# Kernel optimization log

Measured on AMD Instinct MI355X. Metric: run time of the kernel, lower is better.

## Reference

```python
import jax, jax.numpy as jnp
import numpy as np

L, H, D, V, TMAX = 6, 16, 1024, 32000, 2048
HD = D // H
EPS = 1e-5


def _ln(x, g, b):
    m = jnp.mean(x, axis=-1, keepdims=True)
    v = jnp.var(x, axis=-1, keepdims=True)
    return (x - m) * jax.lax.rsqrt(v + EPS) * g + b


def setup_inputs() -> dict:
    key = jax.random.key(0)
    ks = jax.random.split(key, 16)
    s = 0.02
    inp = {
        'idx': jax.random.randint(ks[0], (2, TMAX), 0, V),
        'targets': jax.random.randint(ks[1], (2, TMAX), 0, V),
        'tok_emb': jax.random.normal(ks[2], (V, D), jnp.float32) * s,
        'pos_emb': jax.random.normal(ks[3], (TMAX, D), jnp.float32) * s,
        'wq': jax.random.normal(ks[4], (L, D, D), jnp.float32) * s,
        'wk': jax.random.normal(ks[5], (L, D, D), jnp.float32) * s,
        'wv': jax.random.normal(ks[6], (L, D, D), jnp.float32) * s,
        'w_proj': jax.random.normal(ks[7], (L, D, D), jnp.float32) * s,
        'b_proj': jnp.zeros((L, D), jnp.float32),
        'w_fc1': jax.random.normal(ks[8], (L, D, 4 * D), jnp.float32) * s,
        'b_fc1': jnp.zeros((L, 4 * D), jnp.float32),
        'w_fc2': jax.random.normal(ks[9], (L, 4 * D, D), jnp.float32) * s,
        'b_fc2': jnp.zeros((L, D), jnp.float32),
        'ln1_g': jnp.ones((L, D), jnp.float32), 'ln1_b': jnp.zeros((L, D), jnp.float32),
        'ln2_g': jnp.ones((L, D), jnp.float32), 'ln2_b': jnp.zeros((L, D), jnp.float32),
        'lnf_g': jnp.ones((D,), jnp.float32), 'lnf_b': jnp.zeros((D,), jnp.float32),
        'w_head': jax.random.normal(ks[10], (D, V), jnp.float32) * s,
        'b_head': jnp.zeros((V,), jnp.float32),
    }
    return inp


def reference(idx, targets, tok_emb, pos_emb, wq, wk, wv, w_proj, b_proj,
              w_fc1, b_fc1, w_fc2, b_fc2, ln1_g, ln1_b, ln2_g, ln2_b,
              lnf_g, lnf_b, w_head, b_head):
    B, T = idx.shape
    x = tok_emb[idx] + pos_emb[:T]  # [B,T,D]
    causal = jnp.tril(jnp.ones((T, T), bool))
    scale = HD ** -0.5
    for l in range(L):
        h = _ln(x, ln1_g[l], ln1_b[l])
        q = (h @ wq[l]).reshape(B, T, H, HD)
        k = (h @ wk[l]).reshape(B, T, H, HD)
        v = (h @ wv[l]).reshape(B, T, H, HD)
        att = jnp.einsum('bqhd,bkhd->bhqk', q, k) * scale
        att = jnp.where(causal, att, -jnp.inf)
        att = jax.nn.softmax(att, axis=-1)  # dropout is identity in eval
        o = jnp.einsum('bhqk,bkhd->bqhd', att, v).reshape(B, T, D)
        x = x + o @ w_proj[l] + b_proj[l]
        h = _ln(x, ln2_g[l], ln2_b[l])
        x = x + jax.nn.relu(h @ w_fc1[l] + b_fc1[l]) @ w_fc2[l] + b_fc2[l]
    x = _ln(x, lnf_g, lnf_b)
    logits = x @ w_head + b_head  # [B,T,V]
    logp = jax.nn.log_softmax(logits, axis=-1)
    nll = -jnp.take_along_axis(logp, targets[..., None], axis=-1)[..., 0]
    loss = jnp.mean(nll)
    return logits, loss
```

## Files before the change

### kernel.cpp

```cpp
#include <hip/hip_runtime.h>

#define LAYERS 6
#define NH 16
#define DIM 1024
#define VOCAB 32000
#define SEQ 2048
#define NBATCH 2
#define HEADD 64
#define NROW (NBATCH*SEQ)
#define FF 4096
#define QKVS 3072
#define NCB (VOCAB/256)
#define LN_EPS 1e-5f

typedef unsigned short bfu;
typedef __attribute__((ext_vector_type(8))) short s16x8;
typedef __attribute__((ext_vector_type(4))) float f32x4;

__device__ __forceinline__ float bf2f(bfu u) { return __uint_as_float(((unsigned)u) << 16); }
__device__ __forceinline__ bfu f2bf(float x) {
  unsigned u = __float_as_uint(x);
  return (bfu)((u + 0x7fffu + ((u >> 16) & 1u)) >> 16);
}

__device__ __forceinline__ void gload16(const void* g, void* l) {
  __builtin_amdgcn_global_load_lds((const __attribute__((address_space(1))) void*)g,
                                   (__attribute__((address_space(3))) void*)l, 16, 0, 0);
}

__device__ __forceinline__ f32x4 mfma32(s16x8 a, s16x8 b, f32x4 c) {
  return __builtin_amdgcn_mfma_f32_16x16x32_bf16(a, b, c, 0, 0, 0);
}

__global__ __launch_bounds__(256) void tkernel(const float* __restrict__ in,
                                               bfu* __restrict__ out, int R, int C) {
  __shared__ bfu tile[32][33];
  int tx = threadIdx.x, ty = threadIdx.y;
  int bx = blockIdx.x * 32, by = blockIdx.y * 32;
#pragma unroll
  for (int i = 0; i < 4; ++i)
    tile[ty + i * 8][tx] = f2bf(in[(size_t)(by + ty + i * 8) * C + bx + tx]);
  __syncthreads();
#pragma unroll
  for (int i = 0; i < 4; ++i)
    out[(size_t)(bx + ty + i * 8) * R + by + tx] = tile[tx][ty + i * 8];
}

__global__ __launch_bounds__(256) void wtrans_kernel(const float* __restrict__ wq,
                                                     const float* __restrict__ wk,
                                                     const float* __restrict__ wv,
                                                     const float* __restrict__ wp,
                                                     const float* __restrict__ w1,
                                                     const float* __restrict__ w2,
                                                     bfu* __restrict__ qkvT,
                                                     bfu* __restrict__ wpT,
                                                     bfu* __restrict__ f1T,
                                                     bfu* __restrict__ f2T) {
  __shared__ bfu tile[32][33];
  int bi = blockIdx.x;
  const float* in; bfu* out; int R, C, id;
  if (bi < 4096) {
    int p = bi >> 10; id = bi & 1023;
    in = p == 0 ? wq : p == 1 ? wk : p == 2 ? wv : wp;
    out = (p == 3) ? wpT : qkvT + (size_t)p * DIM * DIM;
    R = DIM; C = DIM;
  } else if (bi < 8192) {
    id = bi - 4096; in = w1; out = f1T; R = DIM; C = FF;
  } else {
    id = bi - 8192; in = w2; out = f2T; R = FF; C = DIM;
  }
  int nbx = C >> 5;
  int bx = (id % nbx) * 32, by = (id / nbx) * 32;
  int tx = threadIdx.x, ty = threadIdx.y;
#pragma unroll
  for (int i = 0; i < 4; ++i)
    tile[ty + i * 8][tx] = f2bf(in[(size_t)(by + ty + i * 8) * C + bx + tx]);
  __syncthreads();
#pragma unroll
  for (int i = 0; i < 4; ++i)
    out[(size_t)(bx + ty + i * 8) * R + by + tx] = tile[tx][ty + i * 8];
}

__global__ __launch_bounds__(256) void vtrans_kernel(const bfu* __restrict__ qkvb,
                                                     bfu* __restrict__ vT) {
  __shared__ bfu tile[32][33];
  int bh = blockIdx.z;
  int b = bh >> 4, h = bh & 15;
  int t0 = blockIdx.x * 32, d0 = blockIdx.y * 32;
  int tx = threadIdx.x, ty = threadIdx.y;
  const bfu* in = qkvb + (size_t)b * SEQ * QKVS + 2048 + h * HEADD;
#pragma unroll
  for (int i = 0; i < 4; ++i)
    tile[ty + i * 8][tx] = in[(size_t)(t0 + ty + i * 8) * QKVS + d0 + tx];
  __syncthreads();
  bfu* out = vT + ((size_t)bh * HEADD) * SEQ;
#pragma unroll
  for (int i = 0; i < 4; ++i)
    out[(size_t)(d0 + ty + i * 8) * SEQ + t0 + tx] = tile[tx][ty + i * 8];
}

__global__ __launch_bounds__(256) void embed_kernel(const int* __restrict__ idx,
                                                    const float* __restrict__ tok,
                                                    const float* __restrict__ pos,
                                                    float* __restrict__ xf) {
  int row = blockIdx.x;
  int t = row % SEQ;
  int tokid = idx[row];
  int d0 = threadIdx.x * 4;
  float4 tv = *(const float4*)&tok[(size_t)tokid * DIM + d0];
  float4 pv = *(const float4*)&pos[(size_t)t * DIM + d0];
  float4 r;
  r.x = tv.x + pv.x; r.y = tv.y + pv.y; r.z = tv.z + pv.z; r.w = tv.w + pv.w;
  *(float4*)&xf[(size_t)row * DIM + d0] = r;
}

__global__ __launch_bounds__(256) void ln_kernel(const float* __restrict__ xf,
                                                 const float* __restrict__ gw,
                                                 const float* __restrict__ bw,
                                                 bfu* __restrict__ h) {
  int row = blockIdx.x, tid = threadIdx.x;
  const float* xr = xf + (size_t)row * DIM;
  float4 xv4 = ((const float4*)xr)[tid];
  float xv[4] = {xv4.x, xv4.y, xv4.z, xv4.w};
  float s = xv[0] + xv[1] + xv[2] + xv[3];
  float ss = xv[0]*xv[0] + xv[1]*xv[1] + xv[2]*xv[2] + xv[3]*xv[3];
  for (int o = 32; o; o >>= 1) { s += __shfl_xor(s, o); ss += __shfl_xor(ss, o); }
  __shared__ float red[8];
  int wave = tid >> 6;
  if ((tid & 63) == 0) { red[wave * 2] = s; red[wave * 2 + 1] = ss; }
  __syncthreads();
  s  = red[0] + red[2] + red[4] + red[6];
  ss = red[1] + red[3] + red[5] + red[7];
  float mean = s * (1.0f / DIM);
  float var = ss * (1.0f / DIM) - mean * mean;
  float inv = rsqrtf(var + LN_EPS);
  int i0 = tid * 4;
  float4 gv = ((const float4*)gw)[tid];
  float4 bv = ((const float4*)bw)[tid];
  ushort4 hv;
  hv.x = f2bf((xv[0] - mean) * inv * gv.x + bv.x);
  hv.y = f2bf((xv[1] - mean) * inv * gv.y + bv.y);
  hv.z = f2bf((xv[2] - mean) * inv * gv.z + bv.z);
  hv.w = f2bf((xv[3] - mean) * inv * gv.w + bv.w);
  *(ushort4*)(h + (size_t)row * DIM + i0) = hv;
}

template <int MODE>
__global__ __launch_bounds__(256) void gemm_bt(const bfu* __restrict__ A,
                                               const bfu* __restrict__ Bt,
                                               const float* __restrict__ bias,
                                               const float* resid,
                                               void* outp,
                                               int M, int N, int K) {
  __shared__ __align__(16) char sm[32768];
  const int tid = threadIdx.x;
  const int lane = tid & 63, wave = tid >> 6;
  const int c = lane & 15, g = lane >> 4;

  const int gx = gridDim.x, gy = gridDim.y;
  int orig = blockIdx.y * gx + blockIdx.x;
  int cpx = (gx * gy) >> 3;
  int swz = (orig & 7) * cpx + (orig >> 3);
  int by = swz / gx, bx = swz - by * gx;

  const int m0 = by * 128, n0 = bx * 128;
  const int wm = (wave & 1) * 64, wn = (wave >> 1) * 64;
  f32x4 acc[4][4] = {};
  const char* Ac = (const char*)A;
  const char* Bc = (const char*)Bt;
  const size_t stride = (size_t)K * 2;

  const int g1 = tid, g2 = tid + 256;
  const int r1 = g1 >> 2, j1 = g1 & 3;
  const int r2 = g2 >> 2, j2 = g2 & 3;
  const size_t a1 = (size_t)(m0 + r1) * stride + j1 * 16;
  const size_t a2 = (size_t)(m0 + r2) * stride + j2 * 16;
  const size_t b1 = (size_t)(n0 + r1) * stride + j1 * 16;
  const size_t b2 = (size_t)(n0 + r2) * stride + j2 * 16;

  auto STAGE = [&](int kt, int buf) {
    char* base = sm + buf * 16384;
    size_t ko = (size_t)kt * 64;
    gload16(Ac + a1 + ko, base + g1 * 16);
    gload16(Ac + a2 + ko, base + g2 * 16);
    gload16(Bc + b1 + ko, base + 8192 + g1 * 16);
    gload16(Bc + b2 + ko, base + 8192 + g2 * 16);
  };

  const int NT = K >> 5;
  STAGE(0, 0);
  STAGE(1, 1);
  asm volatile("s_waitcnt vmcnt(4)" ::: "memory");
  __builtin_amdgcn_s_barrier();
  __builtin_amdgcn_sched_barrier(0);

  for (int i = 0; i < NT; ++i) {
    const char* base = sm + (i & 1) * 16384;
    s16x8 af[4], bfr[4];
#pragma unroll
    for (int mi = 0; mi < 4; ++mi)
      af[mi] = *(const s16x8*)(base + (wm + mi * 16 + c) * 64 + g * 16);
#pragma unroll
    for (int ni = 0; ni < 4; ++ni)
      bfr[ni] = *(const s16x8*)(base + 8192 + (wn + ni * 16 + c) * 64 + g * 16);
    asm volatile("s_waitcnt lgkmcnt(0)" ::: "memory");
    __builtin_amdgcn_sched_barrier(0);
    __builtin_amdgcn_s_barrier();
    __builtin_amdgcn_sched_barrier(0);
    if (i + 2 < NT) STAGE(i + 2, i & 1);
    __builtin_amdgcn_s_setprio(1);
#pragma unroll
    for (int mi = 0; mi < 4; ++mi)
#pragma unroll
      for (int ni = 0; ni < 4; ++ni)
        acc[mi][ni] = mfma32(af[mi], bfr[ni], acc[mi][ni]);
    __builtin_amdgcn_s_setprio(0);
    if (i < NT - 2) {
      asm volatile("s_waitcnt vmcnt(4)" ::: "memory");
      __builtin_amdgcn_s_barrier();
      __builtin_amdgcn_sched_barrier(0);
    } else if (i == NT - 2) {
      asm volatile("s_waitcnt vmcnt(0)" ::: "memory");
      __builtin_amdgcn_s_barrier();
      __builtin_amdgcn_sched_barrier(0);
    }
  }

#pragma unroll
  for (int mi = 0; mi < 4; ++mi) {
#pragma unroll
    for (int ni = 0; ni < 4; ++ni) {
      int col = n0 + wn + ni * 16 + c;
      float bv = bias ? bias[col] : 0.0f;
#pragma unroll
      for (int jj = 0; jj < 4; ++jj) {
        int row = m0 + wm + mi * 16 + g * 4 + jj;
        float val = acc[mi][ni][jj] + bv;
        size_t oi = (size_t)row * N + col;
        if (MODE == 1) val = fmaxf(val, 0.0f);
        if (MODE == 2)      ((float*)outp)[oi] = resid[oi] + val;
        else if (MODE == 3) ((float*)outp)[oi] = val;
        else                ((bfu*)outp)[oi] = f2bf(val);
      }
    }
  }
}

template <int MODE>
__global__ __launch_bounds__(1024) void gemm1024(const bfu* __restrict__ A,
                                                 const bfu* __restrict__ Bt,
                                                 const float* __restrict__ bias,
                                                 const float* resid,
                                                 void* outp,
                                                 int M, int N, int K,
                                                 int colchunk,
                                                 float* __restrict__ pmax,
                                                 float* __restrict__ psum) {
  extern __shared__ char smem[];
  const int tid = threadIdx.x;
  const int lane = tid & 63, w = tid >> 6;
  const int c = lane & 15, g = lane >> 4;

  const int gx = gridDim.x, gy = gridDim.y;
  int orig = blockIdx.y * gx + blockIdx.x;
  int cpx = (gx * gy) >> 3;
  int swz = (orig & 7) * cpx + (orig >> 3);
  int bx, by;
  if (colchunk) { bx = swz / gy; by = swz - bx * gy; }
  else          { by = swz / gx; bx = swz - by * gx; }
  const int m0 = by * 256, n0 = bx * 256;

  const int wrow = w >> 2, wcol = w & 3;
  const size_t gstr = (size_t)K * 2;
  const char* Ag = (const char*)A + (size_t)m0 * gstr;
  const char* Bg = (const char*)Bt + (size_t)n0 * gstr;

  int srow0 = tid >> 3, scg0 = (tid & 7) ^ (srow0 & 7);
  int srow1 = (tid + 1024) >> 3, scg1 = (tid & 7) ^ (srow1 & 7);
  const size_t ga0 = (size_t)srow0 * gstr + scg0 * 16;
  const size_t ga1 = (size_t)srow1 * gstr + scg1 * 16;

  auto STAGE = [&](int kt, int buf) {
    char* base = smem + buf * 65536;
    size_t ko = (size_t)kt * 128;
    gload16(Ag + ga0 + ko, base + w * 1024);
    gload16(Ag + ga1 + ko, base + 16384 + w * 1024);
    gload16(Bg + ga0 + ko, base + 32768 + w * 1024);
    gload16(Bg + ga1 + ko, base + 49152 + w * 1024);
  };

  const int NT = K >> 6;
  f32x4 acc[4][4] = {};

  STAGE(0, 0);
  STAGE(1, 1);
  asm volatile("s_waitcnt vmcnt(4)" ::: "memory");
  __builtin_amdgcn_s_barrier();
  __builtin_amdgcn_sched_barrier(0);

  const int rsw = (c & 7) << 4;
  const int off0 = (g * 16) ^ rsw;
  const int off1 = (64 + g * 16) ^ rsw;

  for (int i = 0; i < NT; ++i) {
    const char* ldsA = smem + (i & 1) * 65536 + (wrow * 64 + c) * 128;
    const char* ldsB = smem + (i & 1) * 65536 + 32768 + (wcol * 64 + c) * 128;
    s16x8 a[4], b[4];
#pragma unroll
    for (int mi = 0; mi < 4; ++mi) a[mi] = *(const s16x8*)(ldsA + mi * 2048 + off0);
#pragma unroll
    for (int ni = 0; ni < 4; ++ni) b[ni] = *(const s16x8*)(ldsB + ni * 2048 + off0);
    __builtin_amdgcn_s_setprio(1);
#pragma unroll
    for (int mi = 0; mi < 4; ++mi)
#pragma unroll
      for (int ni = 0; ni < 4; ++ni)
        acc[mi][ni] = mfma32(a[mi], b[ni], acc[mi][ni]);
    __builtin_amdgcn_s_setprio(0);
#pragma unroll
    for (int mi = 0; mi < 4; ++mi) a[mi] = *(const s16x8*)(ldsA + mi * 2048 + off1);
#pragma unroll
    for (int ni = 0; ni < 4; ++ni) b[ni] = *(const s16x8*)(ldsB + ni * 2048 + off1);
    asm volatile("s_waitcnt lgkmcnt(0)" ::: "memory");
    __builtin_amdgcn_sched_barrier(0);
    __builtin_amdgcn_s_barrier();
    __builtin_amdgcn_sched_barrier(0);
    if (i + 2 < NT) STAGE(i + 2, i & 1);
    __builtin_amdgcn_s_setprio(1);
#pragma unroll
    for (int mi = 0; mi < 4; ++mi)
#pragma unroll
      for (int ni = 0; ni < 4; ++ni)
        acc[mi][ni] = mfma32(a[mi], b[ni], acc[mi][ni]);
    __builtin_amdgcn_s_setprio(0);
    if (i < NT - 2) {
      asm volatile("s_waitcnt vmcnt(4)" ::: "memory");
      __builtin_amdgcn_s_barrier();
      __builtin_amdgcn_sched_barrier(0);
    } else if (i == NT - 2) {
      asm volatile("s_waitcnt vmcnt(0)" ::: "memory");
      __builtin_amdgcn_s_barrier();
      __builtin_amdgcn_sched_barrier(0);
    }
  }

  if (MODE != 4) {
#pragma unroll
    for (int mi = 0; mi < 4; ++mi) {
#pragma unroll
      for (int ni = 0; ni < 4; ++ni) {
        int col = n0 + wcol * 64 + ni * 16 + c;
        float bv = bias ? bias[col] : 0.0f;
#pragma unroll
        for (int jj = 0; jj < 4; ++jj) {
          int row = m0 + wrow * 64 + mi * 16 + g * 4 + jj;
          float val = acc[mi][ni][jj] + bv;
          size_t oi = (size_t)row * N + col;
          if (MODE == 1) val = fmaxf(val, 0.0f);
          else if (MODE == 2) { ((float*)outp)[oi] = resid[oi] + val; continue; }
          if (MODE == 3) ((float*)outp)[oi] = val;
          else           ((bfu*)outp)[oi] = f2bf(val);
        }
      }
    }
  } else {
    float* sred = (float*)(smem + 131072);
    const int ncb = N >> 8;
    float bvv[4]; int colv[4];
#pragma unroll
    for (int ni = 0; ni < 4; ++ni) {
      colv[ni] = n0 + wcol * 64 + ni * 16 + c;
      bvv[ni] = bias ? bias[colv[ni]] : 0.0f;
    }
#pragma unroll
    for (int mi = 0; mi < 4; ++mi) {
#pragma unroll
      for (int jj = 0; jj < 4; ++jj) {
        int row = m0 + wrow * 64 + mi * 16 + g * 4 + jj;
        float v[4];
#pragma unroll
        for (int ni = 0; ni < 4; ++ni) {
          v[ni] = acc[mi][ni][jj] + bvv[ni];
          ((float*)outp)[(size_t)row * N + colv[ni]] = v[ni];
        }
        float mx = fmaxf(fmaxf(v[0], v[1]), fmaxf(v[2], v[3]));
        float sm = __expf(v[0] - mx) + __expf(v[1] - mx) + __expf(v[2] - mx) + __expf(v[3] - mx);
#pragma unroll
        for (int off = 1; off < 16; off <<= 1) {
          float om = __shfl_xor(mx, off), os = __shfl_xor(sm, off);
          float nm = fmaxf(mx, om);
          sm = sm * __expf(mx - nm) + os * __expf(om - nm);
          mx = nm;
        }
        if (c == 0) {
          int r64 = mi * 16 + g * 4 + jj;
          sred[(w * 64 + r64) * 2 + 0] = mx;
          sred[(w * 64 + r64) * 2 + 1] = sm;
        }
      }
    }
    __syncthreads();
    if (tid < 256) {
      int wr = tid >> 6, r64 = tid & 63;
      float M2 = -3.0e38f, S2 = 0.0f;
#pragma unroll
      for (int wc2 = 0; wc2 < 4; ++wc2) {
        float m_i = sred[((wr * 4 + wc2) * 64 + r64) * 2 + 0];
        float s_i = sred[((wr * 4 + wc2) * 64 + r64) * 2 + 1];
        float nm = fmaxf(M2, m_i);
        S2 = S2 * __expf(M2 - nm) + s_i * __expf(m_i - nm);
        M2 = nm;
      }
      size_t pi = (size_t)(m0 + tid) * ncb + bx;
      pmax[pi] = M2;
      psum[pi] = S2;
    }
  }
}

__global__ __launch_bounds__(256) void attn_kernel(const bfu* __restrict__ qkv,
                                                   const bfu* __restrict__ vT,
                                                   bfu* __restrict__ o) {
  __shared__ __align__(16) bfu Ks[64 * 64];
  __shared__ __align__(16) bfu Vt[64 * 64];
  __shared__ __align__(16) bfu Plds[4 * 16 * 32];
  const int tid = threadIdx.x;
  const int lane = tid & 63, w = tid >> 6;
  const int c = lane & 15, g = lane >> 4;
  const int qt = blockIdx.x, hh = blockIdx.y, b = blockIdx.z;
  const int q0 = qt * 64 + w * 16;
  const float SENT = -1e30f;
  const size_t rowb = (size_t)b * SEQ;

  const size_t qbase = (rowb + q0 + c) * QKVS + hh * HEADD + g * 8;
  s16x8 qf0 = *(const s16x8*)&qkv[qbase];
  s16x8 qf1 = *(const s16x8*)&qkv[qbase + 32];
  const bfu* Kg = qkv + 1024 + hh * HEADD;
  const bfu* vTb = vT + (size_t)(b * NH + hh) * HEADD * SEQ;
  bfu* Pw = Plds + w * 512;

  const int srow = tid >> 3;
  const int sgr = (tid & 7) ^ (srow & 7);
  const int cw = c & 7;

  f32x4 oacc[4] = {};
  float mrun = SENT, lrun = 0.0f;

  const int nkt = qt + 1;
  for (int kt = 0; kt < nkt; ++kt) {
    const int k0 = kt * 64;
    __syncthreads();
#pragma unroll
    for (int p = 0; p < 2; ++p) {
      int r = p * 32 + srow;
      gload16(Kg + (rowb + k0 + r) * QKVS + sgr * 8, (char*)Ks + p * 4096 + w * 1024);
      gload16(vTb + (size_t)r * SEQ + k0 + sgr * 8, (char*)Vt + p * 4096 + w * 1024);
    }
    asm volatile("s_waitcnt vmcnt(0)" ::: "memory");
    __syncthreads();

#pragma unroll
    for (int s = 0; s < 2; ++s) {
      const int k0s = k0 + s * 32;
      if (k0s <= q0 + 15) {
        const char* Kb = (const char*)Ks + (size_t)(s * 32 + c) * 128;
        s16x8 kf00 = *(const s16x8*)(Kb + ((g ^ cw) * 16));
        s16x8 kf01 = *(const s16x8*)(Kb + (((4 + g) ^ cw) * 16));
        s16x8 kf10 = *(const s16x8*)(Kb + 16 * 128 + ((g ^ cw) * 16));
        s16x8 kf11 = *(const s16x8*)(Kb + 16 * 128 + (((4 + g) ^ cw) * 16));
        f32x4 s0 = {}, s1 = {};
        s0 = mfma32(kf00, qf0, s0); s0 = mfma32(kf01, qf1, s0);
        s1 = mfma32(kf10, qf0, s1); s1 = mfma32(kf11, qf1, s1);

        float sv[8];
#pragma unroll
        for (int jj = 0; jj < 4; ++jj) {
          int ka = k0s + g * 4 + jj, kb = ka + 16;
          sv[jj]     = (ka <= q0 + c) ? s0[jj] * 0.125f : SENT;
          sv[4 + jj] = (kb <= q0 + c) ? s1[jj] * 0.125f : SENT;
        }
        float tmax = sv[0];
#pragma unroll
        for (int i = 1; i < 8; ++i) tmax = fmaxf(tmax, sv[i]);
        tmax = fmaxf(tmax, __shfl_xor(tmax, 16));
        tmax = fmaxf(tmax, __shfl_xor(tmax, 32));
        float mnew = fmaxf(mrun, tmax);
        float alpha = __expf(mrun - mnew);
        float p[8], psm = 0.0f;
#pragma unroll
        for (int i = 0; i < 8; ++i) { p[i] = __expf(sv[i] - mnew); psm += p[i]; }
        psm += __shfl_xor(psm, 16);
        psm += __shfl_xor(psm, 32);
        lrun = lrun * alpha + psm;
        mrun = mnew;

        ushort4 w0; w0.x = f2bf(p[0]); w0.y = f2bf(p[1]); w0.z = f2bf(p[2]); w0.w = f2bf(p[3]);
        ushort4 w1; w1.x = f2bf(p[4]); w1.y = f2bf(p[5]); w1.z = f2bf(p[6]); w1.w = f2bf(p[7]);
        *(ushort4*)&Pw[c * 32 + g * 4] = w0;
        *(ushort4*)&Pw[c * 32 + 16 + g * 4] = w1;
        asm volatile("s_waitcnt lgkmcnt(0)" ::: "memory");
        __builtin_amdgcn_sched_barrier(0);

        float aq[4];
#pragma unroll
        for (int jj = 0; jj < 4; ++jj) aq[jj] = __shfl(alpha, g * 4 + jj);

        ushort4 ra = *(const ushort4*)&Pw[c * 32 + g * 8];
        ushort4 rb = *(const ushort4*)&Pw[c * 32 + g * 8 + 4];
        s16x8 pa = {(short)ra.x, (short)ra.y, (short)ra.z, (short)ra.w,
                    (short)rb.x, (short)rb.y, (short)rb.z, (short)rb.w};

#pragma unroll
        for (int dg = 0; dg < 4; ++dg) {
          s16x8 vf = *(const s16x8*)((const char*)Vt + (size_t)(dg * 16 + c) * 128 +
                                     (((s * 4 + g) ^ cw) * 16));
#pragma unroll
          for (int jj = 0; jj < 4; ++jj) oacc[dg][jj] *= aq[jj];
          oacc[dg] = mfma32(pa, vf, oacc[dg]);
        }
      }
    }
  }

  float lq[4];
#pragma unroll
  for (int jj = 0; jj < 4; ++jj) lq[jj] = __shfl(lrun, g * 4 + jj);
#pragma unroll
  for (int dg = 0; dg < 4; ++dg)
#pragma unroll
    for (int jj = 0; jj < 4; ++jj) {
      size_t oi = (size_t)(rowb + q0 + g * 4 + jj) * DIM + hh * HEADD + dg * 16 + c;
      o[oi] = f2bf(oacc[dg][jj] / lq[jj]);
    }
}

__global__ __launch_bounds__(64) void nll_finish(const float* __restrict__ pmax,
                                                 const float* __restrict__ psum,
                                                 const float* __restrict__ logits,
                                                 const int* __restrict__ tgt,
                                                 float* __restrict__ nll) {
  int row = blockIdx.x, lane = threadIdx.x;
  const float* pm = pmax + (size_t)row * NCB;
  const float* ps = psum + (size_t)row * NCB;
  float m = -3.0e38f, s = 0.0f;
  if (lane < NCB) { m = pm[lane]; s = ps[lane]; }
  int i2 = lane + 64;
  if (i2 < NCB) {
    float m2 = pm[i2], s2 = ps[i2];
    float nm = fmaxf(m, m2);
    s = s * __expf(m - nm) + s2 * __expf(m2 - nm);
    m = nm;
  }
#pragma unroll
  for (int off = 32; off; off >>= 1) {
    float om = __shfl_xor(m, off), os = __shfl_xor(s, off);
    float nm = fmaxf(m, om);
    s = s * __expf(m - nm) + os * __expf(om - nm);
    m = nm;
  }
  if (lane == 0)
    nll[row] = (m + __logf(s)) - logits[(size_t)row * VOCAB + tgt[row]];
}

__global__ __launch_bounds__(256) void loss_kernel(const float* __restrict__ nll,
                                                   float* __restrict__ out) {
  float s = 0.0f;
  for (int i = threadIdx.x; i < NROW; i += 256) s += nll[i];
  for (int off = 32; off; off >>= 1) s += __shfl_xor(s, off);
  __shared__ float r[4];
  int wave = threadIdx.x >> 6;
  if ((threadIdx.x & 63) == 0) r[wave] = s;
  __syncthreads();
  if (threadIdx.x == 0) out[(size_t)NROW * VOCAB] = (r[0] + r[1] + r[2] + r[3]) * (1.0f / NROW);
}

extern "C" void kernel_launch(void* const* d_in, const int* in_sizes, int n_in,
                              void* d_out, int out_size, void* d_ws, size_t ws_size,
                              hipStream_t stream) {
  (void)in_sizes; (void)n_in; (void)out_size;
  const int* idx       = (const int*)d_in[0];
  const int* targets   = (const int*)d_in[1];
  const float* tok_emb = (const float*)d_in[2];
  const float* pos_emb = (const float*)d_in[3];
  const float* wq      = (const float*)d_in[4];
  const float* wk      = (const float*)d_in[5];
  const float* wv      = (const float*)d_in[6];
  const float* w_proj  = (const float*)d_in[7];
  const float* b_proj  = (const float*)d_in[8];
  const float* w_fc1   = (const float*)d_in[9];
  const float* b_fc1   = (const float*)d_in[10];
  const float* w_fc2   = (const float*)d_in[11];
  const float* b_fc2   = (const float*)d_in[12];
  const float* ln1_g   = (const float*)d_in[13];
  const float* ln1_b   = (const float*)d_in[14];
  const float* ln2_g   = (const float*)d_in[15];
  const float* ln2_b   = (const float*)d_in[16];
  const float* lnf_g   = (const float*)d_in[17];
  const float* lnf_b   = (const float*)d_in[18];
  const float* w_head  = (const float*)d_in[19];
  const float* b_head  = (const float*)d_in[20];

  char* ws = (char*)d_ws;
  size_t off = 0;
  auto alloc = [&](size_t bytes) {
    char* p = ws + off;
    off += (bytes + 255) & ~(size_t)255;
    return p;
  };
  float* xf   = (float*)alloc((size_t)NROW * DIM * 4);
  bfu* hbuf   = (bfu*)alloc((size_t)NROW * DIM * 2);
  bfu* qkvb   = (bfu*)alloc((size_t)NROW * QKVS * 2);
  bfu* ob     = (bfu*)alloc((size_t)NROW * DIM * 2);
  bfu* ub     = (bfu*)alloc((size_t)NROW * FF * 2);
  bfu* vT     = (bfu*)alloc((size_t)NROW * DIM * 2);
  bfu* qkvT   = (bfu*)alloc((size_t)QKVS * DIM * 2);
  bfu* wpT    = (bfu*)alloc((size_t)DIM * DIM * 2);
  bfu* f1T    = (bfu*)alloc((size_t)DIM * FF * 2);
  bfu* f2T    = (bfu*)alloc((size_t)DIM * FF * 2);
  bfu* hT     = (bfu*)alloc((size_t)DIM * VOCAB * 2);
  float* nll  = (float*)alloc((size_t)NROW * 4);
  float* pmax = (float*)alloc((size_t)NROW * NCB * 4);
  float* psum = (float*)alloc((size_t)NROW * NCB * 4);
  if (off > ws_size) return;

  const size_t LDSB = 131072;
  dim3 tb(32, 8);
  tkernel<<<dim3(VOCAB / 32, DIM / 32), tb, 0, stream>>>(w_head, hT, DIM, VOCAB);
  embed_kernel<<<NROW, 256, 0, stream>>>(idx, tok_emb, pos_emb, xf);

  float* logits = (float*)d_out;
  for (int l = 0; l < LAYERS; ++l) {
    const size_t wo = (size_t)l * DIM * DIM, fo = (size_t)l * DIM * FF;
    wtrans_kernel<<<12288, tb, 0, stream>>>(wq + wo, wk + wo, wv + wo, w_proj + wo,
                                            w_fc1 + fo, w_fc2 + fo, qkvT, wpT, f1T, f2T);
    ln_kernel<<<NROW, 256, 0, stream>>>(xf, ln1_g + l * DIM, ln1_b + l * DIM, hbuf);
    gemm_bt<0><<<dim3(QKVS / 128, NROW / 128), 256, 0, stream>>>(
        hbuf, qkvT, nullptr, nullptr, qkvb, NROW, QKVS, DIM);
    vtrans_kernel<<<dim3(SEQ / 32, HEADD / 32, NBATCH * NH), tb, 0, stream>>>(qkvb, vT);
    attn_kernel<<<dim3(SEQ / 64, NH, NBATCH), 256, 0, stream>>>(qkvb, vT, ob);
    gemm_bt<2><<<dim3(DIM / 128, NROW / 128), 256, 0, stream>>>(
        ob, wpT, b_proj + l * DIM, xf, xf, NROW, DIM, DIM);
    ln_kernel<<<NROW, 256, 0, stream>>>(xf, ln2_g + l * DIM, ln2_b + l * DIM, hbuf);
    gemm1024<1><<<dim3(FF / 256, NROW / 256), 1024, LDSB, stream>>>(
        hbuf, f1T, b_fc1 + l * FF, nullptr, ub, NROW, FF, DIM, 0, nullptr, nullptr);
    gemm_bt<2><<<dim3(DIM / 128, NROW / 128), 256, 0, stream>>>(
        ub, f2T, b_fc2 + l * DIM, xf, xf, NROW, DIM, FF);
  }

  ln_kernel<<<NROW, 256, 0, stream>>>(xf, lnf_g, lnf_b, hbuf);
  gemm1024<4><<<dim3(VOCAB / 256, NROW / 256), 1024, LDSB + 8192, stream>>>(
      hbuf, hT, b_head, nullptr, logits, NROW, VOCAB, DIM, 1, pmax, psum);
  nll_finish<<<NROW, 64, 0, stream>>>(pmax, psum, logits, targets, nll);
  loss_kernel<<<1, 256, 0, stream>>>(nll, logits);
}
```

Measured before the change: 2.293 ms.

## Double-buffer K/V tiles in attention and simplify head softmax reduction

The attention kernel now keeps two LDS buffers for K and V tiles and prefetches the tile two steps ahead, using vmcnt-based waits so global loads overlap with MFMA compute. This replaces the load-then-full-wait pattern on every iteration. The head GEMM's row-softmax partial reduction now does a max shuffle-reduce first and then a sum shuffle-reduce, instead of an online merge that needed extra exps per step. Doubling the K/V buffers increases LDS use, and the hand-written waitcnt and barrier logic is fragile.

```diff
diff --git a/kernel.cpp b/kernel.cpp
--- a/kernel.cpp
+++ b/kernel.cpp
@@ -384,14 +384,12 @@
           ((float*)outp)[(size_t)row * N + colv[ni]] = v[ni];
         }
         float mx = fmaxf(fmaxf(v[0], v[1]), fmaxf(v[2], v[3]));
-        float sm = __expf(v[0] - mx) + __expf(v[1] - mx) + __expf(v[2] - mx) + __expf(v[3] - mx);
-#pragma unroll
-        for (int off = 1; off < 16; off <<= 1) {
-          float om = __shfl_xor(mx, off), os = __shfl_xor(sm, off);
-          float nm = fmaxf(mx, om);
-          sm = sm * __expf(mx - nm) + os * __expf(om - nm);
-          mx = nm;
-        }
+#pragma unroll
+        for (int off = 1; off < 16; off <<= 1) mx = fmaxf(mx, __shfl_xor(mx, off));
+        float sm = __expf(v[0] - mx) + __expf(v[1] - mx) +
+                   __expf(v[2] - mx) + __expf(v[3] - mx);
+#pragma unroll
+        for (int off = 1; off < 16; off <<= 1) sm += __shfl_xor(sm, off);
         if (c == 0) {
           int r64 = mi * 16 + g * 4 + jj;
           sred[(w * 64 + r64) * 2 + 0] = mx;
@@ -421,8 +419,8 @@
 __global__ __launch_bounds__(256) void attn_kernel(const bfu* __restrict__ qkv,
                                                    const bfu* __restrict__ vT,
                                                    bfu* __restrict__ o) {
-  __shared__ __align__(16) bfu Ks[64 * 64];
-  __shared__ __align__(16) bfu Vt[64 * 64];
+  __shared__ __align__(16) bfu Ks[2][64 * 64];
+  __shared__ __align__(16) bfu Vt[2][64 * 64];
   __shared__ __align__(16) bfu Plds[4 * 16 * 32];
   const int tid = threadIdx.x;
   const int lane = tid & 63, w = tid >> 6;
@@ -447,23 +445,33 @@
   float mrun = SENT, lrun = 0.0f;
 
   const int nkt = qt + 1;
+
+  auto STAGE = [&](int kt, int buf) {
+    const int k0 = kt * 64;
+#pragma unroll
+    for (int p = 0; p < 2; ++p) {
+      int r = p * 32 + srow;
+      gload16(Kg + (rowb + k0 + r) * QKVS + sgr * 8, (char*)Ks[buf] + p * 4096 + w * 1024);
+      gload16(vTb + (size_t)r * SEQ + k0 + sgr * 8, (char*)Vt[buf] + p * 4096 + w * 1024);
+    }
+  };
+
+  STAGE(0, 0);
+  if (nkt > 1) STAGE(1, 1);
+  if (nkt > 1) asm volatile("s_waitcnt vmcnt(4)" ::: "memory");
+  else         asm volatile("s_waitcnt vmcnt(0)" ::: "memory");
+  __builtin_amdgcn_s_barrier();
+  __builtin_amdgcn_sched_barrier(0);
+
   for (int kt = 0; kt < nkt; ++kt) {
     const int k0 = kt * 64;
-    __syncthreads();
-#pragma unroll
-    for (int p = 0; p < 2; ++p) {
-      int r = p * 32 + srow;
-      gload16(Kg + (rowb + k0 + r) * QKVS + sgr * 8, (char*)Ks + p * 4096 + w * 1024);
-      gload16(vTb + (size_t)r * SEQ + k0 + sgr * 8, (char*)Vt + p * 4096 + w * 1024);
-    }
-    asm volatile("s_waitcnt vmcnt(0)" ::: "memory");
-    __syncthreads();
+    const int buf = kt & 1;
 
 #pragma unroll
     for (int s = 0; s < 2; ++s) {
       const int k0s = k0 + s * 32;
       if (k0s <= q0 + 15) {
-        const char* Kb = (const char*)Ks + (size_t)(s * 32 + c) * 128;
+        const char* Kb = (const char*)Ks[buf] + (size_t)(s * 32 + c) * 128;
         s16x8 kf00 = *(const s16x8*)(Kb + ((g ^ cw) * 16));
         s16x8 kf01 = *(const s16x8*)(Kb + (((4 + g) ^ cw) * 16));
         s16x8 kf10 = *(const s16x8*)(Kb + 16 * 128 + ((g ^ cw) * 16));
@@ -512,13 +520,25 @@
 
 #pragma unroll
         for (int dg = 0; dg < 4; ++dg) {
-          s16x8 vf = *(const s16x8*)((const char*)Vt + (size_t)(dg * 16 + c) * 128 +
+          s16x8 vf = *(const s16x8*)((const char*)Vt[buf] + (size_t)(dg * 16 + c) * 128 +
                                      (((s * 4 + g) ^ cw) * 16));
 #pragma unroll
           for (int jj = 0; jj < 4; ++jj) oacc[dg][jj] *= aq[jj];
           oacc[dg] = mfma32(pa, vf, oacc[dg]);
         }
       }
+    }
+
+    asm volatile("s_waitcnt lgkmcnt(0)" ::: "memory");
+    __builtin_amdgcn_sched_barrier(0);
+    __builtin_amdgcn_s_barrier();
+    __builtin_amdgcn_sched_barrier(0);
+    if (kt + 2 < nkt) STAGE(kt + 2, buf);
+    if (kt + 1 < nkt) {
+      if (kt + 2 < nkt) asm volatile("s_waitcnt vmcnt(4)" ::: "memory");
+      else              asm volatile("s_waitcnt vmcnt(0)" ::: "memory");
+      __builtin_amdgcn_s_barrier();
+      __builtin_amdgcn_sched_barrier(0);
     }
   }
 
```

After: 2.297 ms. No clear change (+0.1%).
